# Performance work log

Hardware: AMD Instinct MI355X
Metric: run time of the kernel (lower is better)

## Reference

```python
import jax, jax.numpy as jnp
import numpy as np

D = 512
H = 16
DH = D // H
N = 1024
R0 = 10.0
K_ITER = 20
LAM = 1.0


def _ln(x, w=None, b=None, eps=1e-5):
    m = x.mean(-1, keepdims=True)
    v = ((x - m) ** 2).mean(-1, keepdims=True)
    y = (x - m) * jax.lax.rsqrt(v + eps)
    if w is not None:
        y = y * w + b
    return y


def setup_inputs() -> dict:
    key = jax.random.key(0)
    ks = jax.random.split(key, 24)
    s = 1.0 / np.sqrt(D)
    inp = {
        'h': jax.random.normal(ks[0], (N, D), jnp.float32),
        'x_res': jax.random.normal(ks[1], (N, 3), jnp.float32) * 5.0,
        'mu': jax.random.uniform(ks[2], (H, N), jnp.float32, 0.1, 1.0),
        'nu': jax.random.uniform(ks[3], (H, N), jnp.float32, 0.1, 1.0),
        'log_u_prev': jnp.zeros((H, N), jnp.float32),
        'log_v_prev': jnp.zeros((H, N), jnp.float32),
        'w_rel_res': jax.random.normal(ks[4], (H, N, N), jnp.float32) * 0.1,
        'w_dist': jax.random.uniform(ks[5], (H,), jnp.float32),
        'pos_bins': jax.random.randint(ks[6], (N, N), 0, 68),
        'geo_gate': jax.random.uniform(ks[7], (H,), jnp.float32),
        'ln_attn_w': jnp.ones((D,), jnp.float32),
        'ln_attn_b': jnp.zeros((D,), jnp.float32),
        'Wq': jax.random.normal(ks[8], (D, D), jnp.float32) * s,
        'Wk': jax.random.normal(ks[9], (D, D), jnp.float32) * s,
        'Wv': jax.random.normal(ks[10], (D, D), jnp.float32) * s,
        'Wg': jax.random.normal(ks[11], (D, D), jnp.float32) * s,
        'Wo': jax.random.normal(ks[12], (D, D), jnp.float32) * s,
        'gamma': jax.random.normal(ks[13], (H,), jnp.float32) * 0.01,
        'ln_ff_w': jnp.ones((D,), jnp.float32),
        'ln_ff_b': jnp.zeros((D,), jnp.float32),
        'W1': jax.random.normal(ks[14], (D, 4 * D), jnp.float32) * s,
        'W3': jax.random.normal(ks[15], (D, 4 * D), jnp.float32) * s,
        'W2': jax.random.normal(ks[16], (4 * D, D), jnp.float32) / np.sqrt(4 * D),
    }
    return inp


def reference(h, x_res, mu, nu, log_u_prev, log_v_prev, w_rel_res, w_dist,
              pos_bins, geo_gate, ln_attn_w, ln_attn_b, Wq, Wk, Wv, Wg, Wo,
              gamma, ln_ff_w, ln_ff_b, W1, W3, W2):
    n = h.shape[0]
    h_n = _ln(h, ln_attn_w, ln_attn_b)
    # projections -> (H, N, d_h)
    Q = (h_n @ Wq).reshape(n, H, DH).transpose(1, 0, 2)
    K = (h_n @ Wk).reshape(n, H, DH).transpose(1, 0, 2)
    V = (h_n @ Wv).reshape(n, H, DH).transpose(1, 0, 2)
    G = (h_n @ Wg).reshape(n, H, DH).transpose(1, 0, 2)
    Q_ln = _ln(Q)
    K_ln = _ln(K)
    content = -jnp.einsum('hid,hjd->hij', Q_ln, K_ln) / np.sqrt(DH)
    pos_bias = w_rel_res  # precomputed (H, N, N)
    d2 = ((x_res[:, None, :] - x_res[None, :, :]) ** 2).sum(-1)
    dist = jnp.sqrt(jnp.maximum(d2, 1e-12))
    f_dist = dist / (R0 + dist)
    eff_w = geo_gate * w_dist
    C = content + pos_bias + eff_w[:, None, None] * f_dist[None]
    # log-domain unbalanced Sinkhorn, per-head eps
    eps_h = jnp.array([0.5] * 4 + [1.0] * 4 + [2.0] * 4 + [4.0] * 4, jnp.float32)
    eps_b = eps_h[:, None, None]
    fac = (LAM / (LAM + eps_h))[:, None]  # (H, 1)
    log_mu = jnp.log(jnp.clip(mu, 1e-8))
    log_nu = jnp.log(jnp.clip(nu, 1e-8))
    M = -C / eps_b  # (H, N, N)

    def step(carry, _):
        lu, lv = carry
        lu = fac * (log_mu - jax.nn.logsumexp(M + lv[:, None, :], axis=2))
        lv = fac * (log_nu - jax.nn.logsumexp(M + lu[:, :, None], axis=1))
        return (lu, lv), None

    (log_u, log_v), _ = jax.lax.scan(jax.checkpoint(step),
                                     (log_u_prev, log_v_prev), None,
                                     length=K_ITER)
    # transport plan and outputs
    T = jnp.exp(M + log_u[:, :, None] + log_v[:, None, :])
    T_norm = T / (T.sum(-1, keepdims=True) + 1e-8)
    o = jax.nn.sigmoid(G) * jnp.einsum('hij,hjd->hid', T_norm, V)
    o = o.transpose(1, 0, 2).reshape(n, D)
    h = h + o @ Wo
    x_centroid = jnp.einsum('hij,jc->hic', T_norm, x_res)  # (H, N, 3)
    delta = x_res[None] - x_centroid
    x_res = x_res + jnp.einsum('h,hnc->nc', gamma, delta)
    # SwiGLU FFN
    ff = _ln(h, ln_ff_w, ln_ff_b)
    h = h + (jax.nn.silu(ff @ W1) * (ff @ W3)) @ W2
    return h, x_res, log_u, log_v
```

## Files before the change

### kernel.cpp

```cpp
#include <hip/hip_runtime.h>
#include <math.h>

#define NTOK 1024
#define DDIM 512

using short8 = __attribute__((ext_vector_type(8))) short;
using f32x4  = __attribute__((ext_vector_type(4))) float;

__device__ __forceinline__ float4 ld4(const float* p){ return *(const float4*)p; }
__device__ __forceinline__ void st4(float* p, float4 v){ *(float4*)p = v; }
__device__ __forceinline__ unsigned short bf16r(float x) {
  unsigned int u = __float_as_uint(x);
  u += 0x7fffu + ((u >> 16) & 1u);
  return (unsigned short)(u >> 16);
}
__device__ __forceinline__ float bf16f(unsigned short h) {
  return __uint_as_float(((unsigned int)h) << 16);
}
__device__ __forceinline__ f32x4 mfma16(short8 a, short8 b, f32x4 c) {
  return __builtin_amdgcn_mfma_f32_16x16x32_bf16(a, b, c, 0, 0, 0);
}

__global__ __launch_bounds__(256) void ln_rows(const float* __restrict__ x,
    const float* __restrict__ w, const float* __restrict__ b, float* __restrict__ y) {
  int row = blockIdx.x, t = threadIdx.x;
  const float* xr = x + ((size_t)row << 9);
  float v0 = xr[t], v1 = xr[t + 256];
  float s = v0 + v1, q = v0*v0 + v1*v1;
  #pragma unroll
  for (int off = 1; off < 64; off <<= 1) { s += __shfl_xor(s, off); q += __shfl_xor(q, off); }
  __shared__ float ls[4], lq[4], mb[2];
  int wv = t >> 6;
  if ((t & 63) == 0) { ls[wv] = s; lq[wv] = q; }
  __syncthreads();
  if (t == 0) {
    float S = ls[0]+ls[1]+ls[2]+ls[3];
    float Q = lq[0]+lq[1]+lq[2]+lq[3];
    float m = S * (1.f/512.f);
    float var = Q * (1.f/512.f) - m*m;
    mb[0] = m; mb[1] = 1.f / sqrtf(var + 1e-5f);
  }
  __syncthreads();
  float m = mb[0], inv = mb[1];
  float* yr = y + ((size_t)row << 9);
  yr[t]       = (v0 - m) * inv * w[t] + b[t];
  yr[t + 256] = (v1 - m) * inv * w[t + 256] + b[t + 256];
}

struct C4 {
  const float *S0, *S1, *S2, *S3;
  unsigned short *D0, *D1, *D2, *D3;
};
__global__ __launch_bounds__(256) void convT(C4 p, int K, int N) {
  __shared__ unsigned short Th[64][68];
  __shared__ unsigned short Tl[64][68];
  int z = blockIdx.z;
  const float* src = (z==0)?p.S0:(z==1)?p.S1:(z==2)?p.S2:p.S3;
  unsigned short* dst = (z==0)?p.D0:(z==1)?p.D1:(z==2)?p.D2:p.D3;
  int nt = blockIdx.x << 6, kt = blockIdx.y << 6;
  int t = threadIdx.x;
  int r = t >> 4, c4 = (t & 15) << 2;
  #pragma unroll
  for (int pp = 0; pp < 4; ++pp) {
    int kk = r + (pp << 4);
    float4 v = ld4(src + (size_t)(kt + kk) * N + nt + c4);
    float vv[4] = {v.x, v.y, v.z, v.w};
    #pragma unroll
    for (int i = 0; i < 4; ++i) {
      unsigned short h = bf16r(vv[i]);
      Th[c4 + i][kk] = h;
      Tl[c4 + i][kk] = bf16r(vv[i] - bf16f(h));
    }
  }
  __syncthreads();
  size_t loff = (size_t)N * K;
  #pragma unroll
  for (int pp = 0; pp < 4; ++pp) {
    int nn = r + (pp << 4);
    ushort4 oh, ol;
    oh.x = Th[nn][c4]; oh.y = Th[nn][c4+1]; oh.z = Th[nn][c4+2]; oh.w = Th[nn][c4+3];
    ol.x = Tl[nn][c4]; ol.y = Tl[nn][c4+1]; ol.z = Tl[nn][c4+2]; ol.w = Tl[nn][c4+3];
    *(ushort4*)(dst + (size_t)(nt + nn) * K + kt + c4) = oh;
    *(ushort4*)(dst + loff + (size_t)(nt + nn) * K + kt + c4) = ol;
  }
}

struct P4 {
  const unsigned short *W0, *W1, *W2, *W3;
  float *C0, *C1, *C2, *C3;
};
template<int MODE>
__global__ __launch_bounds__(256) void gemm_mfma(const float* __restrict__ A,
    P4 p, int Kd, int Nd, int kwin) {
  __shared__ unsigned short Ash[64][72];
  __shared__ unsigned short Asl[64][72];
  __shared__ unsigned short Bsh[64][72];
  __shared__ unsigned short Bsl[64][72];
  int t = threadIdx.x;
  int z = blockIdx.z;
  const unsigned short* W = (z==0)?p.W0:(z==1)?p.W1:(z==2)?p.W2:p.W3;
  float* C = (z==0)?p.C0:(z==1)?p.C1:(z==2)?p.C2:p.C3;
  const unsigned short* Wl = W + (size_t)Nd * Kd;
  int bm = blockIdx.y << 6, bn = blockIdx.x << 6;
  int wid = t >> 6, lane = t & 63;
  int wm = wid >> 1, wn = wid & 1;
  int lr = lane & 15, lk = lane >> 4;
  int r0 = t >> 3, ks = (t & 7) << 3;
  int kbeg = kwin ? z * kwin : 0;
  int kend = kwin ? kbeg + kwin : Kd;
  f32x4 acc[2][2];
  #pragma unroll
  for (int i = 0; i < 2; ++i)
    #pragma unroll
    for (int j = 0; j < 2; ++j)
      #pragma unroll
      for (int r = 0; r < 4; ++r) acc[i][j][r] = 0.f;
  for (int k0 = kbeg; k0 < kend; k0 += 64) {
    float4 a00 = ld4(A + (size_t)(bm + r0) * Kd + k0 + ks);
    float4 a01 = ld4(A + (size_t)(bm + r0) * Kd + k0 + ks + 4);
    float4 a10 = ld4(A + (size_t)(bm + r0 + 32) * Kd + k0 + ks);
    float4 a11 = ld4(A + (size_t)(bm + r0 + 32) * Kd + k0 + ks + 4);
    uint4 b0h = *(const uint4*)(W  + (size_t)(bn + r0) * Kd + k0 + ks);
    uint4 b1h = *(const uint4*)(W  + (size_t)(bn + r0 + 32) * Kd + k0 + ks);
    uint4 b0l = *(const uint4*)(Wl + (size_t)(bn + r0) * Kd + k0 + ks);
    uint4 b1l = *(const uint4*)(Wl + (size_t)(bn + r0 + 32) * Kd + k0 + ks);
    __syncthreads();
    {
      float va[8] = {a00.x,a00.y,a00.z,a00.w,a01.x,a01.y,a01.z,a01.w};
      short8 h8, l8;
      #pragma unroll
      for (int i = 0; i < 8; ++i) {
        unsigned short h = bf16r(va[i]);
        h8[i] = (short)h; l8[i] = (short)bf16r(va[i] - bf16f(h));
      }
      *(short8*)&Ash[r0][ks] = h8;
      *(short8*)&Asl[r0][ks] = l8;
    }
    {
      float va[8] = {a10.x,a10.y,a10.z,a10.w,a11.x,a11.y,a11.z,a11.w};
      short8 h8, l8;
      #pragma unroll
      for (int i = 0; i < 8; ++i) {
        unsigned short h = bf16r(va[i]);
        h8[i] = (short)h; l8[i] = (short)bf16r(va[i] - bf16f(h));
      }
      *(short8*)&Ash[r0 + 32][ks] = h8;
      *(short8*)&Asl[r0 + 32][ks] = l8;
    }
    *(uint4*)&Bsh[r0][ks] = b0h;
    *(uint4*)&Bsh[r0 + 32][ks] = b1h;
    *(uint4*)&Bsl[r0][ks] = b0l;
    *(uint4*)&Bsl[r0 + 32][ks] = b1l;
    __syncthreads();
    #pragma unroll
    for (int s = 0; s < 2; ++s) {
      short8 ah0 = *(const short8*)&Ash[wm*32 + lr][s*32 + lk*8];
      short8 ah1 = *(const short8*)&Ash[wm*32 + 16 + lr][s*32 + lk*8];
      short8 al0 = *(const short8*)&Asl[wm*32 + lr][s*32 + lk*8];
      short8 al1 = *(const short8*)&Asl[wm*32 + 16 + lr][s*32 + lk*8];
      short8 bh0 = *(const short8*)&Bsh[wn*32 + lr][s*32 + lk*8];
      short8 bh1 = *(const short8*)&Bsh[wn*32 + 16 + lr][s*32 + lk*8];
      short8 bl0 = *(const short8*)&Bsl[wn*32 + lr][s*32 + lk*8];
      short8 bl1 = *(const short8*)&Bsl[wn*32 + 16 + lr][s*32 + lk*8];
      acc[0][0] = mfma16(ah0, bh0, acc[0][0]);
      acc[0][1] = mfma16(ah0, bh1, acc[0][1]);
      acc[1][0] = mfma16(ah1, bh0, acc[1][0]);
      acc[1][1] = mfma16(ah1, bh1, acc[1][1]);
      acc[0][0] = mfma16(al0, bh0, acc[0][0]);
      acc[0][1] = mfma16(al0, bh1, acc[0][1]);
      acc[1][0] = mfma16(al1, bh0, acc[1][0]);
      acc[1][1] = mfma16(al1, bh1, acc[1][1]);
      acc[0][0] = mfma16(ah0, bl0, acc[0][0]);
      acc[0][1] = mfma16(ah0, bl1, acc[0][1]);
      acc[1][0] = mfma16(ah1, bl0, acc[1][0]);
      acc[1][1] = mfma16(ah1, bl1, acc[1][1]);
    }
  }
  #pragma unroll
  for (int fm = 0; fm < 2; ++fm)
    #pragma unroll
    for (int fn = 0; fn < 2; ++fn) {
      int n = bn + wn*32 + fn*16 + lr;
      #pragma unroll
      for (int r = 0; r < 4; ++r) {
        int m = bm + wm*32 + fm*16 + lk*4 + r;
        float v = acc[fm][fn][r];
        if (MODE == 0) {
          if (z < 3) C[(((size_t)(n >> 5) << 10) + m) * 32 + (n & 31)] = v;
          else       C[(size_t)m * Nd + n] = v;
        } else {
          C[(size_t)m * Nd + n] = v;
        }
      }
    }
}

__global__ __launch_bounds__(256) void qk_ln(float* __restrict__ Q, float* __restrict__ K) {
  float* P = blockIdx.y ? K : Q;
  int t = threadIdx.x;
  int row = blockIdx.x * 8 + (t >> 5);
  int l = t & 31;
  float* p = P + ((size_t)row << 5);
  float x = p[l];
  float s = x, q = x*x;
  #pragma unroll
  for (int off = 16; off; off >>= 1) { s += __shfl_xor(s, off, 32); q += __shfl_xor(q, off, 32); }
  float m = s * (1.f/32.f);
  float var = q * (1.f/32.f) - m*m;
  float inv = 1.f / sqrtf(var + 1e-5f);
  p[l] = (x - m) * inv;
}

__global__ __launch_bounds__(256) void build_M(const float* __restrict__ Qln,
    const float* __restrict__ Kln, const float* __restrict__ wrel,
    const float* __restrict__ xres, const float* __restrict__ wdist,
    const float* __restrict__ ggate, short* __restrict__ Mq) {
  int jt = blockIdx.x, it = blockIdx.y, h = blockIdx.z;
  int t = threadIdx.x;
  __shared__ float Qs[64][44], Ks[64][44];
  __shared__ float xi[64][4], xj[64][4];
  #pragma unroll
  for (int rep = 0; rep < 2; ++rep) {
    int idx = t + (rep << 8);
    int rr = idx >> 3, dq = (idx & 7) << 2;
    st4(&Qs[rr][dq], ld4(Qln + ((((size_t)h << 10) + (it << 6) + rr) << 5) + dq));
    st4(&Ks[rr][dq], ld4(Kln + ((((size_t)h << 10) + (jt << 6) + rr) << 5) + dq));
  }
  if (t < 64) {
    int gi = (it << 6) + t, gj = (jt << 6) + t;
    xi[t][0] = xres[gi*3]; xi[t][1] = xres[gi*3+1]; xi[t][2] = xres[gi*3+2];
    xj[t][0] = xres[gj*3]; xj[t][1] = xres[gj*3+1]; xj[t][2] = xres[gj*3+2];
  }
  __syncthreads();
  int g = h >> 2;
  float inv_eps = 2.0f / (float)(1 << g);
  float effw = ggate[h] * wdist[h];
  int tr = t >> 4, tc = t & 15;
  float acc[4][4] = {};
  #pragma unroll
  for (int d0 = 0; d0 < 32; d0 += 4) {
    float4 q4[4], k4[4];
    #pragma unroll
    for (int a = 0; a < 4; ++a) q4[a] = ld4(&Qs[(tr << 2) + a][d0]);
    #pragma unroll
    for (int bq = 0; bq < 4; ++bq) k4[bq] = ld4(&Ks[(tc << 2) + bq][d0]);
    #pragma unroll
    for (int a = 0; a < 4; ++a)
      #pragma unroll
      for (int bq = 0; bq < 4; ++bq)
        acc[a][bq] += q4[a].x*k4[bq].x + q4[a].y*k4[bq].y + q4[a].z*k4[bq].z + q4[a].w*k4[bq].w;
  }
  const float is32 = 0.17677669529663687f;
  #pragma unroll
  for (int a = 0; a < 4; ++a) {
    int il = (tr << 2) + a;
    int i = (it << 6) + il;
    float xa0 = xi[il][0], xa1 = xi[il][1], xa2 = xi[il][2];
    size_t base = ((size_t)h << 20) + ((size_t)i << 10) + (jt << 6) + (tc << 2);
    float4 w4 = ld4(wrel + base);
    short o16[4];
    #pragma unroll
    for (int bq = 0; bq < 4; ++bq) {
      int jl = (tc << 2) + bq;
      float dx = xa0 - xj[jl][0], dy = xa1 - xj[jl][1], dz = xa2 - xj[jl][2];
      float d2 = dx*dx + dy*dy + dz*dz;
      float dist = sqrtf(fmaxf(d2, 1e-12f));
      float f = dist / (10.0f + dist);
      float wv = (bq==0)?w4.x:(bq==1)?w4.y:(bq==2)?w4.z:w4.w;
      float m = (acc[a][bq] * is32 - wv - effw * f) * inv_eps;
      o16[bq] = (short)__float2int_rn(fminf(fmaxf(m * 256.f, -32000.f), 32000.f));
    }
    short4 q4o; q4o.x = o16[0]; q4o.y = o16[1]; q4o.z = o16[2]; q4o.w = o16[3];
    *(short4*)(Mq + base) = q4o;
  }
}

__global__ __launch_bounds__(256) void sink_iter8(const short* __restrict__ Mq,
    const float* __restrict__ lvb, const float* __restrict__ mu,
    float* __restrict__ lu_out, float* __restrict__ part) {
  __shared__ float lds[4][1024];
  __shared__ float logmu[16];
  int bt = blockIdx.x, h = blockIdx.y;
  int t = threadIdx.x, w = t >> 6, lane = t & 63;
  float eps = 0.5f * (float)(1 << (h >> 2));
  float fac = 1.f / (1.f + eps);
  const float qs = 1.f / 256.f;
  int rowbase = bt << 4;
  if (t < 16) logmu[t] = __logf(fmaxf(mu[(h << 10) + rowbase + t], 1e-8f));
  const short* Mh = Mq + ((size_t)h << 20);
  int ib = rowbase + (w << 2);
  short8 qa[4], qb[4];
  #pragma unroll
  for (int k = 0; k < 4; ++k) {
    const short* row = Mh + ((size_t)(ib + k) << 10) + (lane << 3);
    qa[k] = *(const short8*)row;
    qb[k] = *(const short8*)(row + 512);
  }
  float4 lv4[2][2], env[2][2];
  #pragma unroll
  for (int c = 0; c < 2; ++c) {
    const float* lp = lvb + (h << 10) + (c << 9) + (lane << 3);
    lv4[c][0] = ld4(lp);
    lv4[c][1] = ld4(lp + 4);
    #pragma unroll
    for (int hv = 0; hv < 2; ++hv) {
      env[c][hv].x = __expf(-lv4[c][hv].x); env[c][hv].y = __expf(-lv4[c][hv].y);
      env[c][hv].z = __expf(-lv4[c][hv].z); env[c][hv].w = __expf(-lv4[c][hv].w);
    }
  }
  float4 colacc[2][2];
  #pragma unroll
  for (int c = 0; c < 2; ++c)
    #pragma unroll
    for (int hv = 0; hv < 2; ++hv) colacc[c][hv] = make_float4(0.f,0.f,0.f,0.f);
  #pragma unroll
  for (int k = 0; k < 4; ++k) {
    short8 q0 = qa[k], q1 = qb[k];
    float4 e[2][2];
    e[0][0].x = __expf((float)q0[0]*qs + lv4[0][0].x);
    e[0][0].y = __expf((float)q0[1]*qs + lv4[0][0].y);
    e[0][0].z = __expf((float)q0[2]*qs + lv4[0][0].z);
    e[0][0].w = __expf((float)q0[3]*qs + lv4[0][0].w);
    e[0][1].x = __expf((float)q0[4]*qs + lv4[0][1].x);
    e[0][1].y = __expf((float)q0[5]*qs + lv4[0][1].y);
    e[0][1].z = __expf((float)q0[6]*qs + lv4[0][1].z);
    e[0][1].w = __expf((float)q0[7]*qs + lv4[0][1].w);
    e[1][0].x = __expf((float)q1[0]*qs + lv4[1][0].x);
    e[1][0].y = __expf((float)q1[1]*qs + lv4[1][0].y);
    e[1][0].z = __expf((float)q1[2]*qs + lv4[1][0].z);
    e[1][0].w = __expf((float)q1[3]*qs + lv4[1][0].w);
    e[1][1].x = __expf((float)q1[4]*qs + lv4[1][1].x);
    e[1][1].y = __expf((float)q1[5]*qs + lv4[1][1].y);
    e[1][1].z = __expf((float)q1[6]*qs + lv4[1][1].z);
    e[1][1].w = __expf((float)q1[7]*qs + lv4[1][1].w);
    float racc = ((e[0][0].x + e[0][0].y) + (e[0][0].z + e[0][0].w))
               + ((e[0][1].x + e[0][1].y) + (e[0][1].z + e[0][1].w))
               + ((e[1][0].x + e[1][0].y) + (e[1][0].z + e[1][0].w))
               + ((e[1][1].x + e[1][1].y) + (e[1][1].z + e[1][1].w));
    #pragma unroll
    for (int off = 1; off < 64; off <<= 1) racc += __shfl_xor(racc, off);
    float lu = fac * (logmu[(w << 2) + k] - __logf(racc));
    if (lane == 0) lu_out[(h << 10) + ib + k] = lu;
    float s1 = __expf(lu);
    #pragma unroll
    for (int c = 0; c < 2; ++c)
      #pragma unroll
      for (int hv = 0; hv < 2; ++hv) {
        colacc[c][hv].x += s1 * (e[c][hv].x * env[c][hv].x);
        colacc[c][hv].y += s1 * (e[c][hv].y * env[c][hv].y);
        colacc[c][hv].z += s1 * (e[c][hv].z * env[c][hv].z);
        colacc[c][hv].w += s1 * (e[c][hv].w * env[c][hv].w);
      }
  }
  #pragma unroll
  for (int c = 0; c < 2; ++c) {
    st4(&lds[w][(c << 9) + (lane << 3)], colacc[c][0]);
    st4(&lds[w][(c << 9) + (lane << 3) + 4], colacc[c][1]);
  }
  __syncthreads();
  #pragma unroll
  for (int c = 0; c < 4; ++c) {
    int j = t + (c << 8);
    float v = (lds[0][j] + lds[1][j]) + (lds[2][j] + lds[3][j]);
    part[(((size_t)(h << 6) + bt) << 10) + j] = v;
  }
}

__global__ __launch_bounds__(256) void sink_fin(const float* __restrict__ part,
    const float* __restrict__ nu, float* __restrict__ lvb) {
  int cx = blockIdx.x, h = blockIdx.y;
  int t = threadIdx.x;
  float eps = 0.5f * (float)(1 << (h >> 2));
  float fac = 1.f / (1.f + eps);
  int j = (cx << 8) + t;
  float sum = 0.f;
  #pragma unroll 16
  for (int b = 0; b < 64; ++b)
    sum += part[(((size_t)(h << 6) + b) << 10) + j];
  float lv = fac * (__logf(fmaxf(nu[(h << 10) + j], 1e-8f)) - __logf(sum));
  lvb[(h << 10) + j] = lv;
}

__global__ __launch_bounds__(256) void attn_out_v4(const short* __restrict__ Mq,
    const float* __restrict__ lu_g, const float* __restrict__ lv_g,
    const float* __restrict__ V, const float* __restrict__ G,
    const float* __restrict__ xres, float* __restrict__ o_buf, float* __restrict__ xc) {
  __shared__ unsigned short eslab[32][1032];
  __shared__ float lv_s[1024];
  __shared__ float lu_s[32];
  __shared__ float Vs[64][40];
  int rb = blockIdx.x, h = blockIdx.y;
  int t = threadIdx.x;
  int rowbase = rb << 5;
  ((float4*)lv_s)[t] = ld4(lv_g + (h << 10) + (t << 2));
  if (t < 32) lu_s[t] = lu_g[(h << 10) + rowbase + t];
  __syncthreads();
  const short* Mh = Mq + ((size_t)h << 20) + ((size_t)rowbase << 10);
  const float qs = 1.f / 256.f;
  #pragma unroll
  for (int rep = 0; rep < 16; ++rep) {
    int idx = (rep << 8) + t;
    int rr = idx >> 7, c8 = (idx & 127) << 3;
    short8 m8 = *(const short8*)(Mh + ((size_t)rr << 10) + c8);
    float lur = lu_s[rr];
    short8 e8;
    #pragma unroll
    for (int i = 0; i < 8; ++i)
      e8[i] = (short)bf16r(__expf((float)m8[i] * qs + lur + lv_s[c8 + i]));
    *(short8*)&eslab[rr][c8] = e8;
  }
  int r = t >> 3, cg = t & 7;
  float accO[4] = {0.f, 0.f, 0.f, 0.f};
  float rs = 0.f, accX = 0.f;
  for (int jt = 0; jt < 16; ++jt) {
    __syncthreads();
    {
      int vr = t >> 2, dq = (t & 3) << 3;
      const float* vp = V + ((((size_t)h << 10) + (jt << 6) + vr) << 5) + dq;
      st4(&Vs[vr][dq], ld4(vp));
      st4(&Vs[vr][dq + 4], ld4(vp + 4));
    }
    if (t < 64) {
      int j = (jt << 6) + t;
      Vs[t][32] = xres[j*3]; Vs[t][33] = xres[j*3+1]; Vs[t][34] = xres[j*3+2];
    }
    __syncthreads();
    const unsigned short* erow = &eslab[r][jt << 6];
    #pragma unroll 8
    for (int jj = 0; jj < 64; ++jj) {
      float e = bf16f(erow[jj]);
      float4 v4 = ld4(&Vs[jj][cg << 2]);
      accO[0] += e*v4.x; accO[1] += e*v4.y; accO[2] += e*v4.z; accO[3] += e*v4.w;
      rs += e;
      accX += e * Vs[jj][32 + cg];
    }
  }
  float inv = 1.f / (rs + 1e-8f);
  int i = rowbase + r;
  size_t ga = ((size_t)i << 9) + (h << 5) + (cg << 2);
  float4 g4 = ld4(G + ga);
  float4 o;
  o.x = accO[0]*inv / (1.f + __expf(-g4.x));
  o.y = accO[1]*inv / (1.f + __expf(-g4.y));
  o.z = accO[2]*inv / (1.f + __expf(-g4.z));
  o.w = accO[3]*inv / (1.f + __expf(-g4.w));
  st4(o_buf + ga, o);
  if (cg < 3)
    xc[((size_t)((h << 10) + i)) * 3 + cg] = accX * inv;
}

__global__ void x_update(const float* __restrict__ xres, const float* __restrict__ xc,
    const float* __restrict__ gamma, float* __restrict__ xout) {
  int idx = blockIdx.x * 256 + threadIdx.x;
  if (idx >= 3072) return;
  float x = xres[idx];
  float s = x;
  #pragma unroll
  for (int hh = 0; hh < 16; ++hh) s += gamma[hh] * (x - xc[(size_t)hh * 3072 + idx]);
  xout[idx] = s;
}

__global__ __launch_bounds__(256) void silu_mul(const float* __restrict__ P1,
    const float* __restrict__ P3, float* __restrict__ AB) {
  int i = (blockIdx.x * 256 + threadIdx.x) << 2;
  float4 a = ld4(P1 + i), b = ld4(P3 + i);
  float4 o;
  o.x = a.x / (1.f + __expf(-a.x)) * b.x;
  o.y = a.y / (1.f + __expf(-a.y)) * b.y;
  o.z = a.z / (1.f + __expf(-a.z)) * b.z;
  o.w = a.w / (1.f + __expf(-a.w)) * b.w;
  st4(AB + i, o);
}

__global__ __launch_bounds__(256) void add3(const float* __restrict__ a,
    const float* __restrict__ b, const float* __restrict__ c, float* __restrict__ o) {
  int i = (blockIdx.x * 256 + threadIdx.x) << 2;
  float4 va = ld4(a + i), vb = ld4(b + i), vc = ld4(c + i);
  st4(o + i, make_float4(va.x+vb.x+vc.x, va.y+vb.y+vc.y, va.z+vb.z+vc.z, va.w+vb.w+vc.w));
}

extern "C" void kernel_launch(void* const* d_in, const int* in_sizes, int n_in,
                              void* d_out, int out_size, void* d_ws, size_t ws_size,
                              hipStream_t stream) {
  const float* h_in    = (const float*)d_in[0];
  const float* x_res   = (const float*)d_in[1];
  const float* mu      = (const float*)d_in[2];
  const float* nu      = (const float*)d_in[3];
  const float* lv_prev = (const float*)d_in[5];
  const float* wrel    = (const float*)d_in[6];
  const float* wdist   = (const float*)d_in[7];
  const float* ggate   = (const float*)d_in[9];
  const float* lnaw    = (const float*)d_in[10];
  const float* lnab    = (const float*)d_in[11];
  const float* Wq      = (const float*)d_in[12];
  const float* Wk      = (const float*)d_in[13];
  const float* Wv      = (const float*)d_in[14];
  const float* Wg      = (const float*)d_in[15];
  const float* Wo      = (const float*)d_in[16];
  const float* gamma   = (const float*)d_in[17];
  const float* lnfw    = (const float*)d_in[18];
  const float* lnfb    = (const float*)d_in[19];
  const float* W1      = (const float*)d_in[20];
  const float* W3      = (const float*)d_in[21];
  const float* W2      = (const float*)d_in[22];

  float* out = (float*)d_out;
  float* OUT_H  = out;
  float* OUT_X  = out + 524288;
  float* OUT_LU = out + 527360;
  float* OUT_LV = out + 543744;

  if (ws_size < (size_t)19988480 * sizeof(float)) return;
  float* ws   = (float*)d_ws;
  float* Qb   = ws;
  float* Kb   = ws + 524288;
  float* Vb   = ws + 1048576;
  float* Gb   = ws + 1572864;
  float* Mb   = ws + 2097152;
  float* part = ws + 18874368;
  float* xcb  = ws + 19922944;
  short* Mq   = (short*)Mb;
  float* h_n = Mb;
  unsigned short* WqT = (unsigned short*)(Mb + 524288);
  unsigned short* WkT = (unsigned short*)(Mb + 786432);
  unsigned short* WvT = (unsigned short*)(Mb + 1048576);
  unsigned short* WgT = (unsigned short*)(Mb + 1310720);
  float* P1 = Mb;
  float* P3 = Mb + 2097152;
  float* ABb = Mb + 4194304;
  unsigned short* W1T = (unsigned short*)(Mb + 6291456);
  unsigned short* W3T = (unsigned short*)(Mb + 7340032);
  unsigned short* W2T = (unsigned short*)(Mb + 8388608);
  unsigned short* WoT = (unsigned short*)(Mb + 9437184);
  float* Pa = Mb + 9699328;
  float* Pb = Mb + 10223616;
  float* o_buf = part;
  float* h2  = Qb;
  float* ffb = Kb;

  ln_rows<<<NTOK, 256, 0, stream>>>(h_in, lnaw, lnab, h_n);
  {
    C4 c = { Wq, Wk, Wv, Wg, WqT, WkT, WvT, WgT };
    convT<<<dim3(8, 8, 4), 256, 0, stream>>>(c, 512, 512);
  }
  {
    P4 p = { WqT, WkT, WvT, WgT, Qb, Kb, Vb, Gb };
    gemm_mfma<0><<<dim3(8, 16, 4), 256, 0, stream>>>(h_n, p, 512, 512, 0);
  }
  qk_ln<<<dim3(2048, 2), 256, 0, stream>>>(Qb, Kb);
  build_M<<<dim3(16, 16, 16), 256, 0, stream>>>(Qb, Kb, wrel, x_res, wdist, ggate, Mq);
  hipMemcpyAsync(OUT_LV, lv_prev, 16384 * sizeof(float), hipMemcpyDeviceToDevice, stream);
  for (int it = 0; it < 20; ++it) {
    sink_iter8<<<dim3(64, 16), 256, 0, stream>>>(Mq, OUT_LV, mu, OUT_LU, part);
    sink_fin<<<dim3(4, 16), 256, 0, stream>>>(part, nu, OUT_LV);
  }
  attn_out_v4<<<dim3(32, 16), 256, 0, stream>>>(Mq, OUT_LU, OUT_LV, Vb, Gb, x_res, o_buf, xcb);
  x_update<<<12, 256, 0, stream>>>(x_res, xcb, gamma, OUT_X);

  {
    C4 c = { Wo, nullptr, nullptr, nullptr, WoT, nullptr, nullptr, nullptr };
    convT<<<dim3(8, 8, 1), 256, 0, stream>>>(c, 512, 512);
  }
  {
    C4 c = { W1, W3, nullptr, nullptr, W1T, W3T, nullptr, nullptr };
    convT<<<dim3(32, 8, 2), 256, 0, stream>>>(c, 512, 2048);
  }
  {
    C4 c = { W2, nullptr, nullptr, nullptr, W2T, nullptr, nullptr, nullptr };
    convT<<<dim3(8, 32, 1), 256, 0, stream>>>(c, 2048, 512);
  }
  {
    P4 p = { WoT, WoT, nullptr, nullptr, Pa, Pb, nullptr, nullptr };
    gemm_mfma<1><<<dim3(8, 16, 2), 256, 0, stream>>>(o_buf, p, 512, 512, 256);
  }
  add3<<<512, 256, 0, stream>>>(Pa, Pb, h_in, h2);
  ln_rows<<<NTOK, 256, 0, stream>>>(h2, lnfw, lnfb, ffb);
  {
    P4 p = { W1T, W3T, nullptr, nullptr, P1, P3, nullptr, nullptr };
    gemm_mfma<1><<<dim3(32, 16, 2), 256, 0, stream>>>(ffb, p, 512, 2048, 0);
  }
  silu_mul<<<2048, 256, 0, stream>>>(P1, P3, ABb);
  {
    P4 p = { W2T, W2T, nullptr, nullptr, Pa, Pb, nullptr, nullptr };
    gemm_mfma<1><<<dim3(8, 16, 2), 256, 0, stream>>>(ABb, p, 2048, 512, 1024);
  }
  add3<<<512, 256, 0, stream>>>(Pa, Pb, h2, OUT_H);
}
```

Measured before the change: 478.1 us.

## Compute QK scores in build_M with split-bf16 MFMA and vectorize attn_out reads

The QK layernorm kernel now writes each normalized Q/K value as a high/low bf16 pair. build_M computes the per-head QK^T tile with three bf16 MFMAs (hi*hi, lo*hi, hi*lo) to approximate fp32 accuracy, replacing the scalar FMA loop that went through LDS. Separately, attn_out reads the exponentiated row slab eight bf16 values at a time and pads the V tile in shared memory. The risk is that build_M's stores and its w_rel loads become scalar with the MFMA output layout, so global access is less well coalesced.

Result: faster. 449.2 us (-6.0%).

```diff
diff --git a/kernel.cpp b/kernel.cpp
--- a/kernel.cpp
+++ b/kernel.cpp
@@ -195,12 +195,17 @@
     }
 }
 
-__global__ __launch_bounds__(256) void qk_ln(float* __restrict__ Q, float* __restrict__ K) {
-  float* P = blockIdx.y ? K : Q;
+__global__ __launch_bounds__(256) void qk_ln_split(const float* __restrict__ Q,
+    const float* __restrict__ K, unsigned short* __restrict__ Qh,
+    unsigned short* __restrict__ Ql, unsigned short* __restrict__ Kh,
+    unsigned short* __restrict__ Kl) {
+  const float* P = blockIdx.y ? K : Q;
+  unsigned short* Dh = blockIdx.y ? Kh : Qh;
+  unsigned short* Dl = blockIdx.y ? Kl : Ql;
   int t = threadIdx.x;
   int row = blockIdx.x * 8 + (t >> 5);
   int l = t & 31;
-  float* p = P + ((size_t)row << 5);
+  const float* p = P + ((size_t)row << 5);
   float x = p[l];
   float s = x, q = x*x;
   #pragma unroll
@@ -208,71 +213,81 @@
   float m = s * (1.f/32.f);
   float var = q * (1.f/32.f) - m*m;
   float inv = 1.f / sqrtf(var + 1e-5f);
-  p[l] = (x - m) * inv;
-}
-
-__global__ __launch_bounds__(256) void build_M(const float* __restrict__ Qln,
-    const float* __restrict__ Kln, const float* __restrict__ wrel,
+  float y = (x - m) * inv;
+  unsigned short hi = bf16r(y);
+  Dh[((size_t)row << 5) + l] = hi;
+  Dl[((size_t)row << 5) + l] = bf16r(y - bf16f(hi));
+}
+
+__global__ __launch_bounds__(256) void build_M(const unsigned short* __restrict__ Qh,
+    const unsigned short* __restrict__ Ql, const unsigned short* __restrict__ Kh,
+    const unsigned short* __restrict__ Kl, const float* __restrict__ wrel,
     const float* __restrict__ xres, const float* __restrict__ wdist,
     const float* __restrict__ ggate, short* __restrict__ Mq) {
   int jt = blockIdx.x, it = blockIdx.y, h = blockIdx.z;
   int t = threadIdx.x;
-  __shared__ float Qs[64][44], Ks[64][44];
-  __shared__ float xi[64][4], xj[64][4];
-  #pragma unroll
-  for (int rep = 0; rep < 2; ++rep) {
-    int idx = t + (rep << 8);
-    int rr = idx >> 3, dq = (idx & 7) << 2;
-    st4(&Qs[rr][dq], ld4(Qln + ((((size_t)h << 10) + (it << 6) + rr) << 5) + dq));
-    st4(&Ks[rr][dq], ld4(Kln + ((((size_t)h << 10) + (jt << 6) + rr) << 5) + dq));
-  }
+  __shared__ float xi[64][3], xj[64][3];
   if (t < 64) {
     int gi = (it << 6) + t, gj = (jt << 6) + t;
     xi[t][0] = xres[gi*3]; xi[t][1] = xres[gi*3+1]; xi[t][2] = xres[gi*3+2];
     xj[t][0] = xres[gj*3]; xj[t][1] = xres[gj*3+1]; xj[t][2] = xres[gj*3+2];
   }
+  int wid = t >> 6, lane = t & 63;
+  int wm = wid >> 1, wn = wid & 1;
+  int lr = lane & 15, lk = lane >> 4;
+  size_t hb = ((size_t)h << 10);
+  short8 ah[2], al[2], bh[2], bl[2];
+  #pragma unroll
+  for (int fm = 0; fm < 2; ++fm) {
+    size_t row = hb + (it << 6) + wm*32 + fm*16 + lr;
+    ah[fm] = *(const short8*)(Qh + (row << 5) + lk*8);
+    al[fm] = *(const short8*)(Ql + (row << 5) + lk*8);
+  }
+  #pragma unroll
+  for (int fn = 0; fn < 2; ++fn) {
+    size_t row = hb + (jt << 6) + wn*32 + fn*16 + lr;
+    bh[fn] = *(const short8*)(Kh + (row << 5) + lk*8);
+    bl[fn] = *(const short8*)(Kl + (row << 5) + lk*8);
+  }
+  f32x4 acc[2][2];
+  #pragma unroll
+  for (int i = 0; i < 2; ++i)
+    #pragma unroll
+    for (int j = 0; j < 2; ++j)
+      #pragma unroll
+      for (int r = 0; r < 4; ++r) acc[i][j][r] = 0.f;
+  #pragma unroll
+  for (int fm = 0; fm < 2; ++fm)
+    #pragma unroll
+    for (int fn = 0; fn < 2; ++fn) {
+      acc[fm][fn] = mfma16(ah[fm], bh[fn], acc[fm][fn]);
+      acc[fm][fn] = mfma16(al[fm], bh[fn], acc[fm][fn]);
+      acc[fm][fn] = mfma16(ah[fm], bl[fn], acc[fm][fn]);
+    }
   __syncthreads();
-  int g = h >> 2;
-  float inv_eps = 2.0f / (float)(1 << g);
+  float inv_eps = 2.0f / (float)(1 << (h >> 2));
   float effw = ggate[h] * wdist[h];
-  int tr = t >> 4, tc = t & 15;
-  float acc[4][4] = {};
-  #pragma unroll
-  for (int d0 = 0; d0 < 32; d0 += 4) {
-    float4 q4[4], k4[4];
-    #pragma unroll
-    for (int a = 0; a < 4; ++a) q4[a] = ld4(&Qs[(tr << 2) + a][d0]);
-    #pragma unroll
-    for (int bq = 0; bq < 4; ++bq) k4[bq] = ld4(&Ks[(tc << 2) + bq][d0]);
-    #pragma unroll
-    for (int a = 0; a < 4; ++a)
-      #pragma unroll
-      for (int bq = 0; bq < 4; ++bq)
-        acc[a][bq] += q4[a].x*k4[bq].x + q4[a].y*k4[bq].y + q4[a].z*k4[bq].z + q4[a].w*k4[bq].w;
-  }
   const float is32 = 0.17677669529663687f;
   #pragma unroll
-  for (int a = 0; a < 4; ++a) {
-    int il = (tr << 2) + a;
-    int i = (it << 6) + il;
-    float xa0 = xi[il][0], xa1 = xi[il][1], xa2 = xi[il][2];
-    size_t base = ((size_t)h << 20) + ((size_t)i << 10) + (jt << 6) + (tc << 2);
-    float4 w4 = ld4(wrel + base);
-    short o16[4];
-    #pragma unroll
-    for (int bq = 0; bq < 4; ++bq) {
-      int jl = (tc << 2) + bq;
-      float dx = xa0 - xj[jl][0], dy = xa1 - xj[jl][1], dz = xa2 - xj[jl][2];
-      float d2 = dx*dx + dy*dy + dz*dz;
-      float dist = sqrtf(fmaxf(d2, 1e-12f));
-      float f = dist / (10.0f + dist);
-      float wv = (bq==0)?w4.x:(bq==1)?w4.y:(bq==2)?w4.z:w4.w;
-      float m = (acc[a][bq] * is32 - wv - effw * f) * inv_eps;
-      o16[bq] = (short)__float2int_rn(fminf(fmaxf(m * 256.f, -32000.f), 32000.f));
-    }
-    short4 q4o; q4o.x = o16[0]; q4o.y = o16[1]; q4o.z = o16[2]; q4o.w = o16[3];
-    *(short4*)(Mq + base) = q4o;
-  }
+  for (int fm = 0; fm < 2; ++fm)
+    #pragma unroll
+    for (int fn = 0; fn < 2; ++fn) {
+      int coll = wn*32 + fn*16 + lr;
+      int colg = (jt << 6) + coll;
+      float xj0 = xj[coll][0], xj1 = xj[coll][1], xj2 = xj[coll][2];
+      #pragma unroll
+      for (int i = 0; i < 4; ++i) {
+        int rowl = wm*32 + fm*16 + lk*4 + i;
+        int rowg = (it << 6) + rowl;
+        float dx = xi[rowl][0] - xj0, dy = xi[rowl][1] - xj1, dz = xi[rowl][2] - xj2;
+        float d2 = dx*dx + dy*dy + dz*dz;
+        float dist = sqrtf(fmaxf(d2, 1e-12f));
+        float f = dist / (10.0f + dist);
+        size_t base = ((size_t)h << 20) + ((size_t)rowg << 10) + colg;
+        float m = (acc[fm][fn][i] * is32 - wrel[base] - effw * f) * inv_eps;
+        Mq[base] = (short)__float2int_rn(fminf(fmaxf(m * 256.f, -32000.f), 32000.f));
+      }
+    }
 }
 
 __global__ __launch_bounds__(256) void sink_iter8(const short* __restrict__ Mq,
@@ -381,14 +396,14 @@
   lvb[(h << 10) + j] = lv;
 }
 
-__global__ __launch_bounds__(256) void attn_out_v4(const short* __restrict__ Mq,
+__global__ __launch_bounds__(256) void attn_out_v5(const short* __restrict__ Mq,
     const float* __restrict__ lu_g, const float* __restrict__ lv_g,
     const float* __restrict__ V, const float* __restrict__ G,
     const float* __restrict__ xres, float* __restrict__ o_buf, float* __restrict__ xc) {
   __shared__ unsigned short eslab[32][1032];
   __shared__ float lv_s[1024];
   __shared__ float lu_s[32];
-  __shared__ float Vs[64][40];
+  __shared__ float Vs[64][44];
   int rb = blockIdx.x, h = blockIdx.y;
   int t = threadIdx.x;
   int rowbase = rb << 5;
@@ -426,13 +441,18 @@
     }
     __syncthreads();
     const unsigned short* erow = &eslab[r][jt << 6];
-    #pragma unroll 8
-    for (int jj = 0; jj < 64; ++jj) {
-      float e = bf16f(erow[jj]);
-      float4 v4 = ld4(&Vs[jj][cg << 2]);
-      accO[0] += e*v4.x; accO[1] += e*v4.y; accO[2] += e*v4.z; accO[3] += e*v4.w;
-      rs += e;
-      accX += e * Vs[jj][32 + cg];
+    #pragma unroll
+    for (int j8 = 0; j8 < 8; ++j8) {
+      short8 e8 = *(const short8*)(erow + (j8 << 3));
+      #pragma unroll
+      for (int i = 0; i < 8; ++i) {
+        int jj = (j8 << 3) + i;
+        float e = bf16f((unsigned short)e8[i]);
+        float4 v4 = ld4(&Vs[jj][cg << 2]);
+        accO[0] += e*v4.x; accO[1] += e*v4.y; accO[2] += e*v4.z; accO[3] += e*v4.w;
+        rs += e;
+        accX += e * Vs[jj][32 + cg];
+      }
     }
   }
   float inv = 1.f / (rs + 1e-8f);
@@ -525,6 +545,10 @@
   unsigned short* WkT = (unsigned short*)(Mb + 786432);
   unsigned short* WvT = (unsigned short*)(Mb + 1048576);
   unsigned short* WgT = (unsigned short*)(Mb + 1310720);
+  unsigned short* Qhh = (unsigned short*)(Mb + 8388608);
+  unsigned short* Qll = (unsigned short*)(Mb + 8650752);
+  unsigned short* Khh = (unsigned short*)(Mb + 8912896);
+  unsigned short* Kll = (unsigned short*)(Mb + 9175040);
   float* P1 = Mb;
   float* P3 = Mb + 2097152;
   float* ABb = Mb + 4194304;
@@ -547,14 +571,15 @@
     P4 p = { WqT, WkT, WvT, WgT, Qb, Kb, Vb, Gb };
     gemm_mfma<0><<<dim3(8, 16, 4), 256, 0, stream>>>(h_n, p, 512, 512, 0);
   }
-  qk_ln<<<dim3(2048, 2), 256, 0, stream>>>(Qb, Kb);
-  build_M<<<dim3(16, 16, 16), 256, 0, stream>>>(Qb, Kb, wrel, x_res, wdist, ggate, Mq);
+  qk_ln_split<<<dim3(2048, 2), 256, 0, stream>>>(Qb, Kb, Qhh, Qll, Khh, Kll);
+  build_M<<<dim3(16, 16, 16), 256, 0, stream>>>(Qhh, Qll, Khh, Kll, wrel, x_res,
+                                                wdist, ggate, Mq);
   hipMemcpyAsync(OUT_LV, lv_prev, 16384 * sizeof(float), hipMemcpyDeviceToDevice, stream);
   for (int it = 0; it < 20; ++it) {
     sink_iter8<<<dim3(64, 16), 256, 0, stream>>>(Mq, OUT_LV, mu, OUT_LU, part);
     sink_fin<<<dim3(4, 16), 256, 0, stream>>>(part, nu, OUT_LV);
   }
-  attn_out_v4<<<dim3(32, 16), 256, 0, stream>>>(Mq, OUT_LU, OUT_LV, Vb, Gb, x_res, o_buf, xcb);
+  attn_out_v5<<<dim3(32, 16), 256, 0, stream>>>(Mq, OUT_LU, OUT_LV, Vb, Gb, x_res, o_buf, xcb);
   x_update<<<12, 256, 0, stream>>>(x_res, xcb, gamma, OUT_X);
 
   {
```
